# Kernel tuning notes

Measured on AMD Instinct MI355X. Metric: run time of the kernel, lower is better.

Reference implementation:

```python
import jax, jax.numpy as jnp
import numpy as np
from jax import lax

DN = ('NHWC', 'HWIO', 'NHWC')
N_MEM = 2000  # memory slots
BN_EPS = 1e-3


def _conv(x, w, b):
    # tf.nn.conv2d stride 2, SAME, NHWC / HWIO
    return lax.conv_general_dilated(x, w, (2, 2), 'SAME', dimension_numbers=DN) + b


def _convt(x, w, b):
    # tf.nn.conv2d_transpose; w is TF layout [kh, kw, out_ch, in_ch]
    return lax.conv_transpose(x, w, (2, 2), 'SAME', dimension_numbers=DN,
                              transpose_kernel=True) + b


def _bn(x, g, b):
    # BatchNormalization(training=True): batch statistics over N,H,W
    m = jnp.mean(x, axis=(0, 1, 2))
    v = jnp.var(x, axis=(0, 1, 2))
    return g * (x - m) * lax.rsqrt(v + BN_EPS) + b


def setup_inputs() -> dict:
    key = jax.random.key(0)
    ks = iter(jax.random.split(key, 40))
    def gn(shape, s=0.05):
        return jax.random.normal(next(ks), shape, jnp.float32) * s
    inp = {'x': jax.random.uniform(next(ks), (16, 256, 256, 3), jnp.float32)}
    inp.update(
        w_e1=gn((1, 1, 3, 16)), b_e1=gn((16,)),
        g_bn1=jnp.ones(16, jnp.float32), be_bn1=jnp.zeros(16, jnp.float32),
        w_e2=gn((3, 3, 16, 32)), b_e2=gn((32,)),
        g_bn2=jnp.ones(32, jnp.float32), be_bn2=jnp.zeros(32, jnp.float32),
        w_e3=gn((3, 3, 32, 64)), b_e3=gn((64,)),
        g_bn3=jnp.ones(64, jnp.float32), be_bn3=jnp.zeros(64, jnp.float32),
        w_mem=gn((1, 1, N_MEM, 64)),
        w_d1=gn((3, 3, 32, 64)), b_d1=gn((32,)),
        g_bnt1=jnp.ones(32, jnp.float32), be_bnt1=jnp.zeros(32, jnp.float32),
        w_d2=gn((3, 3, 16, 32)), b_d2=gn((16,)),
        g_bnt2=jnp.ones(16, jnp.float32), be_bnt2=jnp.zeros(16, jnp.float32),
        w_d3=gn((3, 3, 3, 16)), b_d3=gn((3,)),
    )
    return inp


def reference(x, w_e1, b_e1, g_bn1, be_bn1, w_e2, b_e2, g_bn2, be_bn2,
              w_e3, b_e3, g_bn3, be_bn3, w_mem,
              w_d1, b_d1, g_bnt1, be_bnt1, w_d2, b_d2, g_bnt2, be_bnt2,
              w_d3, b_d3):
    # ---- encode ----
    h = jax.nn.relu(_bn(_conv(x, w_e1, b_e1), g_bn1, be_bn1))   # [B,128,128,16]
    h = jax.nn.relu(_bn(_conv(h, w_e2, b_e2), g_bn2, be_bn2))   # [B,64,64,32]
    z = jax.nn.relu(_bn(_conv(h, w_e3, b_e3), g_bn3, be_bn3))   # [B,32,32,64]
    # ---- memory addressing ----
    mem = w_mem[0, 0]                                            # [N, 64]
    num = jnp.einsum('bhwc,nc->bhwn', z, mem)
    den = jnp.einsum('bhwc,nc->bhwn', z * z, mem * mem)
    att = jax.nn.softmax((num + 1e-12) / (den + 1e-12), axis=-1)  # [B,32,32,N]
    d = att - 1.0 / N_MEM                                        # hard shrinkage
    renorm = jnp.clip(jax.nn.relu(d) * att / (jnp.abs(d) + 1e-12),
                      1e-12, 1.0 - 1e-12)
    z_hat = jnp.einsum('bhwn,nc->bhwc', renorm, mem)             # [B,32,32,64]
    # ---- decode ----
    t = jax.nn.relu(_bn(_convt(z_hat, w_d1, b_d1), g_bnt1, be_bnt1))  # [B,64,64,32]
    t = jax.nn.relu(_bn(_convt(t, w_d2, b_d2), g_bnt2, be_bnt2))      # [B,128,128,16]
    x_hat = jnp.clip(_convt(t, w_d3, b_d3), 1e-12, 1.0 - 1e-12)       # [B,256,256,3]
    return x_hat
```

## Files before the change

### kernel.cpp

```cpp
#include <hip/hip_runtime.h>
#include <math.h>

typedef __bf16 bf16x8 __attribute__((ext_vector_type(8)));
typedef __bf16 bf16x4 __attribute__((ext_vector_type(4)));
typedef float  f32x16 __attribute__((ext_vector_type(16)));

static __device__ __forceinline__ f32x16 zero16() {
  f32x16 v;
  #pragma unroll
  for (int i = 0; i < 16; ++i) v[i] = 0.f;
  return v;
}
static __device__ __forceinline__ unsigned int bfbits(__bf16 b) {
  return (unsigned int)__builtin_bit_cast(unsigned short, b);
}
static __device__ __forceinline__ bf16x8 mk8(unsigned int a, unsigned int b,
                                             unsigned int c, unsigned int d) {
  uint4 t; t.x = a; t.y = b; t.z = c; t.w = d;
  return __builtin_bit_cast(bf16x8, t);
}

__global__ __launch_bounds__(256) void k_conv1(const float* __restrict__ x,
    const float* __restrict__ w, const float* __restrict__ b, float* __restrict__ y,
    float* __restrict__ partials) {
  int t = blockIdx.x*256 + threadIdx.x;
  int ox = t & 127, oy = (t >> 7) & 127, bb = t >> 14;
  const float* xp = x + ((size_t)((bb*256 + 2*oy)*256 + 2*ox))*3;
  float x0 = xp[0], x1 = xp[1], x2 = xp[2];
  float4 rg[4];
  float4* yp = (float4*)(y + (size_t)t*16);
  #pragma unroll
  for (int g = 0; g < 4; ++g) {
    float4 r;
    r.x = b[g*4+0] + x0*w[g*4+0] + x1*w[16+g*4+0] + x2*w[32+g*4+0];
    r.y = b[g*4+1] + x0*w[g*4+1] + x1*w[16+g*4+1] + x2*w[32+g*4+1];
    r.z = b[g*4+2] + x0*w[g*4+2] + x1*w[16+g*4+2] + x2*w[32+g*4+2];
    r.w = b[g*4+3] + x0*w[g*4+3] + x1*w[16+g*4+3] + x2*w[32+g*4+3];
    rg[g] = r;
    yp[g] = r;
  }
  float4 s4[4], q4[4];
  #pragma unroll
  for (int g=0; g<4; ++g) {
    s4[g] = rg[g];
    q4[g] = make_float4(rg[g].x*rg[g].x, rg[g].y*rg[g].y, rg[g].z*rg[g].z, rg[g].w*rg[g].w);
  }
  #pragma unroll
  for (int off=1; off<64; off<<=1) {
    #pragma unroll
    for (int g=0; g<4; ++g) {
      s4[g].x += __shfl_xor(s4[g].x, off); s4[g].y += __shfl_xor(s4[g].y, off);
      s4[g].z += __shfl_xor(s4[g].z, off); s4[g].w += __shfl_xor(s4[g].w, off);
      q4[g].x += __shfl_xor(q4[g].x, off); q4[g].y += __shfl_xor(q4[g].y, off);
      q4[g].z += __shfl_xor(q4[g].z, off); q4[g].w += __shfl_xor(q4[g].w, off);
    }
  }
  __shared__ float red[4][32];
  int wv = threadIdx.x >> 6, lane = threadIdx.x & 63;
  if (lane == 0) {
    #pragma unroll
    for (int g=0; g<4; ++g) {
      *(float4*)&red[wv][g*4]      = s4[g];
      *(float4*)&red[wv][16 + g*4] = q4[g];
    }
  }
  __syncthreads();
  if (threadIdx.x < 32)
    partials[(size_t)blockIdx.x*32 + threadIdx.x] =
      red[0][threadIdx.x]+red[1][threadIdx.x]+red[2][threadIdx.x]+red[3][threadIdx.x];
}

template<int C,int CSPLIT>
__global__ __launch_bounds__(256) void k_finalize2(const float* __restrict__ partials, int nblk,
    double inv_n, const float* __restrict__ g, const float* __restrict__ be, float* __restrict__ ss) {
  const int COUTT = C/CSPLIT;
  const int NSTAT = 2*C;
  const int PER = 256/NSTAT;
  __shared__ double red[256];
  int tid = threadIdx.x;
  int st = tid % NSTAT, sub = tid / NSTAT;
  int c = st % C, kind = st / C;
  int cq = c / COUTT, j = c % COUTT;
  int nb = nblk / CSPLIT;
  double acc = 0.0;
  #pragma unroll 4
  for (int i = sub; i < nb; i += PER) {
    int bq = cq + i*CSPLIT;
    acc += (double)partials[(size_t)bq*2*COUTT + kind*COUTT + j];
  }
  red[tid] = acc;
  __syncthreads();
  for (int off = PER>>1; off > 0; off >>= 1) {
    if (sub < off) red[tid] += red[tid + off*NSTAT];
    __syncthreads();
  }
  if (tid < C) {
    double mean = red[tid]*inv_n;
    double var  = red[C+tid]*inv_n - mean*mean;
    float scale = g[tid] * rsqrtf((float)var + 1e-3f);
    float shift = be[tid] - (float)mean*scale;
    ss[tid] = scale; ss[C+tid] = shift;
  }
}

template<int CIN,int COUT,int CSPLIT,int HIN,int HOUT,bool BN>
__global__ __launch_bounds__(256) void k_conv_bn(const float* __restrict__ in,
    const float* __restrict__ w, const float* __restrict__ bias,
    const float* __restrict__ ss, float* __restrict__ y, float* __restrict__ partials) {
  const int COUTT = COUT/CSPLIT;
  const int NW4 = COUTT/4;
  __shared__ float4 wlds[9*CIN*NW4];
  int bid = blockIdx.x;
  int cq  = bid % CSPLIT;
  int pxb = bid / CSPLIT;
  int c0  = cq*COUTT;
  for (int e = threadIdx.x; e < 9*CIN*NW4; e += 256) {
    int r = e / NW4, cg = e % NW4;
    wlds[e] = *(const float4*)(w + (size_t)r*COUT + c0 + cg*4);
  }
  __syncthreads();
  int t0 = pxb*256 + threadIdx.x;
  float4 acc[NW4];
  #pragma unroll
  for (int g=0; g<NW4; ++g) acc[g] = *(const float4*)(bias + c0 + g*4);
  int ox = t0 % HOUT, oy = (t0/HOUT) % HOUT, bb = t0/(HOUT*HOUT);
  #pragma unroll 1
  for (int dy=0; dy<3; ++dy) {
    #pragma unroll 1
    for (int dx=0; dx<3; ++dx) {
      int tap = dy*3+dx;
      int iy = 2*oy + dy, ix = 2*ox + dx;
      if (iy < HIN && ix < HIN) {
        const float* bp = in + ((size_t)(bb*HIN + iy)*HIN + ix)*CIN;
        #pragma unroll
        for (int ci4=0; ci4<CIN/4; ++ci4) {
          float4 v = *(const float4*)(bp + ci4*4);
          if (BN) {
            float4 sc = *(const float4*)(ss + ci4*4);
            float4 sh = *(const float4*)(ss + CIN + ci4*4);
            v.x = fmaxf(0.f, fmaf(v.x, sc.x, sh.x));
            v.y = fmaxf(0.f, fmaf(v.y, sc.y, sh.y));
            v.z = fmaxf(0.f, fmaf(v.z, sc.z, sh.z));
            v.w = fmaxf(0.f, fmaf(v.w, sc.w, sh.w));
          }
          float va[4] = {v.x, v.y, v.z, v.w};
          #pragma unroll
          for (int k=0;k<4;++k) {
            float vk = va[k];
            #pragma unroll
            for (int g=0; g<NW4; ++g) {
              float4 w4 = wlds[(tap*CIN + ci4*4 + k)*NW4 + g];
              acc[g].x = fmaf(vk, w4.x, acc[g].x);
              acc[g].y = fmaf(vk, w4.y, acc[g].y);
              acc[g].z = fmaf(vk, w4.z, acc[g].z);
              acc[g].w = fmaf(vk, w4.w, acc[g].w);
            }
          }
        }
      }
    }
  }
  float4* yp = (float4*)(y + (size_t)t0*COUT + c0);
  #pragma unroll
  for (int g=0;g<NW4;++g) yp[g] = acc[g];
  float4 s4[NW4], q4[NW4];
  #pragma unroll
  for (int g=0; g<NW4; ++g) {
    s4[g] = acc[g];
    q4[g] = make_float4(acc[g].x*acc[g].x, acc[g].y*acc[g].y,
                        acc[g].z*acc[g].z, acc[g].w*acc[g].w);
  }
  #pragma unroll
  for (int off=1; off<64; off<<=1) {
    #pragma unroll
    for (int g=0; g<NW4; ++g) {
      s4[g].x += __shfl_xor(s4[g].x, off); s4[g].y += __shfl_xor(s4[g].y, off);
      s4[g].z += __shfl_xor(s4[g].z, off); s4[g].w += __shfl_xor(s4[g].w, off);
      q4[g].x += __shfl_xor(q4[g].x, off); q4[g].y += __shfl_xor(q4[g].y, off);
      q4[g].z += __shfl_xor(q4[g].z, off); q4[g].w += __shfl_xor(q4[g].w, off);
    }
  }
  __shared__ float red[4][2*COUTT];
  int wv = threadIdx.x >> 6, lane = threadIdx.x & 63;
  if (lane == 0) {
    #pragma unroll
    for (int g=0; g<NW4; ++g) {
      *(float4*)&red[wv][g*4]         = s4[g];
      *(float4*)&red[wv][COUTT + g*4] = q4[g];
    }
  }
  __syncthreads();
  if (threadIdx.x < 2*COUTT)
    partials[(size_t)bid*2*COUTT + threadIdx.x] =
      red[0][threadIdx.x]+red[1][threadIdx.x]+red[2][threadIdx.x]+red[3][threadIdx.x];
}


__global__ __launch_bounds__(256) void k_prep_z(const float* __restrict__ y3,
    const float* __restrict__ ss,
    __bf16* __restrict__ ZH, __bf16* __restrict__ ZL,
    __bf16* __restrict__ Z2H, __bf16* __restrict__ Z2L) {
  int t = blockIdx.x*256 + threadIdx.x;
  float4 v = ((const float4*)y3)[t];
  int c0 = (t*4) & 63;
  float4 sc = *(const float4*)(ss + c0);
  float4 sh = *(const float4*)(ss + 64 + c0);
  float vv[4];
  vv[0] = fmaxf(0.f, fmaf(v.x, sc.x, sh.x));
  vv[1] = fmaxf(0.f, fmaf(v.y, sc.y, sh.y));
  vv[2] = fmaxf(0.f, fmaf(v.z, sc.z, sh.z));
  vv[3] = fmaxf(0.f, fmaf(v.w, sc.w, sh.w));
  bf16x4 h, l, h2, l2;
  #pragma unroll
  for (int i=0;i<4;++i) {
    float f = vv[i];
    __bf16 hb = (__bf16)f;
    h[i] = hb; l[i] = (__bf16)(f - (float)hb);
    float q = f*f;
    __bf16 qb = (__bf16)q;
    h2[i] = qb; l2[i] = (__bf16)(q - (float)qb);
  }
  ((bf16x4*)ZH)[t] = h;  ((bf16x4*)ZL)[t] = l;
  ((bf16x4*)Z2H)[t] = h2; ((bf16x4*)Z2L)[t] = l2;
}

__global__ __launch_bounds__(256) void k_prep_m(const float* __restrict__ mem,
    __bf16* __restrict__ MH, __bf16* __restrict__ ML,
    __bf16* __restrict__ M2H, __bf16* __restrict__ M2L,
    __bf16* __restrict__ MHT, __bf16* __restrict__ MLT) {
  int t = blockIdx.x*256 + threadIdx.x;
  int n = t >> 4, c0 = (t & 15)*4;
  float4 v = make_float4(0.f,0.f,0.f,0.f);
  if (n < 2000) v = *(const float4*)(mem + (size_t)n*64 + c0);
  float vv[4] = {v.x, v.y, v.z, v.w};
  bf16x4 h, l, h2, l2;
  #pragma unroll
  for (int i=0;i<4;++i) {
    float f = vv[i];
    __bf16 hb = (__bf16)f;
    h[i] = hb; l[i] = (__bf16)(f - (float)hb);
    float q = f*f;
    __bf16 qb = (__bf16)q;
    h2[i] = qb; l2[i] = (__bf16)(q - (float)qb);
  }
  *(bf16x4*)(MH  + (size_t)n*64 + c0) = h;
  *(bf16x4*)(ML  + (size_t)n*64 + c0) = l;
  *(bf16x4*)(M2H + (size_t)n*64 + c0) = h2;
  *(bf16x4*)(M2L + (size_t)n*64 + c0) = l2;
  #pragma unroll
  for (int i=0;i<4;++i) {
    MHT[(size_t)(c0+i)*2048 + n] = h[i];
    MLT[(size_t)(c0+i)*2048 + n] = l[i];
  }
}

__global__ __launch_bounds__(256) void k_pass1(
    const __bf16* __restrict__ ZH, const __bf16* __restrict__ ZL,
    const __bf16* __restrict__ Z2H, const __bf16* __restrict__ Z2L,
    const __bf16* __restrict__ MH, const __bf16* __restrict__ ML,
    const __bf16* __restrict__ M2H, const __bf16* __restrict__ M2L,
    float* __restrict__ S32, float* __restrict__ partM, float* __restrict__ partS) {
  int pb = blockIdx.x & 127, chunk = blockIdx.x >> 7;
  int wave = threadIdx.x >> 6, lane = threadIdx.x & 63;
  int p0 = pb*128 + wave*32;
  int col = lane & 31, hi = lane >> 5;
  bf16x8 bzh[4], bzl[4], b2h[4], b2l[4];
  size_t zoff = (size_t)(p0 + col)*64 + hi*8;
  #pragma unroll
  for (int ks=0;ks<4;++ks) {
    bzh[ks] = *(const bf16x8*)(ZH  + zoff + ks*16);
    bzl[ks] = *(const bf16x8*)(ZL  + zoff + ks*16);
    b2h[ks] = *(const bf16x8*)(Z2H + zoff + ks*16);
    b2l[ks] = *(const bf16x8*)(Z2L + zoff + ks*16);
  }
  float m = -3.4e38f, S = 0.f;
  int nbase = chunk*256;
  #pragma unroll 2
  for (int t=0; t<8; ++t) {
    int n0 = nbase + t*32;
    size_t arow = (size_t)(n0 + col)*64 + hi*8;
    f32x16 num = zero16(), den = zero16();
    #pragma unroll
    for (int ks=0;ks<4;++ks) {
      bf16x8 amh = *(const bf16x8*)(MH + arow + ks*16);
      bf16x8 aml = *(const bf16x8*)(ML + arow + ks*16);
      num = __builtin_amdgcn_mfma_f32_32x32x16_bf16(amh, bzh[ks], num, 0,0,0);
      num = __builtin_amdgcn_mfma_f32_32x32x16_bf16(amh, bzl[ks], num, 0,0,0);
      num = __builtin_amdgcn_mfma_f32_32x32x16_bf16(aml, bzh[ks], num, 0,0,0);
      bf16x8 a2h = *(const bf16x8*)(M2H + arow + ks*16);
      bf16x8 a2l = *(const bf16x8*)(M2L + arow + ks*16);
      den = __builtin_amdgcn_mfma_f32_32x32x16_bf16(a2h, b2h[ks], den, 0,0,0);
      den = __builtin_amdgcn_mfma_f32_32x32x16_bf16(a2h, b2l[ks], den, 0,0,0);
      den = __builtin_amdgcn_mfma_f32_32x32x16_bf16(a2l, b2h[ks], den, 0,0,0);
    }
    bool maskt = (n0 + 32 > 2000);
    float sv[16];
    float tmax = -3.4e38f;
    #pragma unroll
    for (int r=0;r<16;++r) {
      float s = (num[r] + 1e-12f) * __builtin_amdgcn_rcpf(den[r] + 1e-12f);
      if (maskt) {
        int nn = n0 + (r&3) + 8*(r>>2) + 4*hi;
        if (nn >= 2000) s = -3.4e38f;
      }
      sv[r] = s;
      tmax = fmaxf(tmax, s);
    }
    {
      size_t sbase = ((size_t)((chunk*8 + t)*16384 + p0 + col)*2 + hi)*16;
      *(float4*)(S32 + sbase)      = make_float4(sv[0], sv[1], sv[2], sv[3]);
      *(float4*)(S32 + sbase + 4)  = make_float4(sv[4], sv[5], sv[6], sv[7]);
      *(float4*)(S32 + sbase + 8)  = make_float4(sv[8], sv[9], sv[10], sv[11]);
      *(float4*)(S32 + sbase + 12) = make_float4(sv[12], sv[13], sv[14], sv[15]);
    }
    float mn = fmaxf(m, tmax);
    float ssum = 0.f;
    #pragma unroll
    for (int r=0;r<16;++r) ssum += __expf(sv[r] - mn);
    S = S*__expf(m - mn) + ssum;
    m = mn;
  }
  float mo = __shfl_xor(m, 32);
  float So = __shfl_xor(S, 32);
  float mf = fmaxf(m, mo);
  float Sf = S*__expf(m - mf) + So*__expf(mo - mf);
  if (lane < 32) {
    int p = p0 + col;
    partM[chunk*16384 + p] = mf;
    partS[chunk*16384 + p] = Sf;
  }
}

__global__ __launch_bounds__(256) void k_pass2(
    const float* __restrict__ S32,
    const __bf16* __restrict__ MHT, const __bf16* __restrict__ MLT,
    const float* __restrict__ partM, const float* __restrict__ partS,
    float* __restrict__ ZP) {
  int pb = blockIdx.x & 127, chunk = blockIdx.x >> 7;
  int wave = threadIdx.x >> 6, lane = threadIdx.x & 63;
  int p0 = pb*128 + wave*32;
  int col = lane & 31, hi = lane >> 5;
  int p = p0 + col;
  float pmv[8];
  float Mp = -3.4e38f;
  #pragma unroll
  for (int c=0;c<8;++c) { pmv[c] = partM[c*16384 + p]; Mp = fmaxf(Mp, pmv[c]); }
  float Ssum = 0.f;
  #pragma unroll
  for (int c=0;c<8;++c) Ssum += partS[c*16384 + p] * __expf(pmv[c] - Mp);
  float CM  = Mp + __logf(Ssum);
  float thr = CM - 7.6009025f;
  f32x16 za0 = zero16(), za1 = zero16();
  int nbase = chunk*256;
  #pragma unroll 2
  for (int t=0; t<8; ++t) {
    int n0 = nbase + t*32;
    size_t sbase = ((size_t)((chunk*8 + t)*16384 + p)*2 + hi)*16;
    float4 sq0 = *(const float4*)(S32 + sbase);
    float4 sq1 = *(const float4*)(S32 + sbase + 4);
    float4 sq2 = *(const float4*)(S32 + sbase + 8);
    float4 sq3 = *(const float4*)(S32 + sbase + 12);
    float sv[16] = {sq0.x,sq0.y,sq0.z,sq0.w, sq1.x,sq1.y,sq1.z,sq1.w,
                    sq2.x,sq2.y,sq2.z,sq2.w, sq3.x,sq3.y,sq3.z,sq3.w};
    float rv[16];
    #pragma unroll
    for (int r=0;r<16;++r) {
      float s = sv[r];
      float att = __expf(s - CM);
      rv[r] = (s > thr) ? att : 0.f;
    }
    unsigned int qh[8];
    #pragma unroll
    for (int qd=0; qd<4; ++qd) {
      #pragma unroll
      for (int pr=0; pr<2; ++pr) {
        float r0 = rv[qd*4 + pr*2], r1 = rv[qd*4 + pr*2 + 1];
        qh[qd*2+pr] = bfbits((__bf16)r0) | (bfbits((__bf16)r1) << 16);
      }
    }
    unsigned int qhp[8];
    #pragma unroll
    for (int i=0;i<8;++i) qhp[i] = (unsigned int)__shfl_xor((int)qh[i], 32);
    bf16x8 f1h = hi ? mk8(qhp[2],qhp[3],qh[2],qh[3]) : mk8(qh[0],qh[1],qhp[0],qhp[1]);
    bf16x8 f2h = hi ? mk8(qhp[6],qhp[7],qh[6],qh[7]) : mk8(qh[4],qh[5],qhp[4],qhp[5]);
    #pragma unroll
    for (int kh=0; kh<2; ++kh) {
      bf16x8 fh = kh ? f2h : f1h;
      size_t bofs = (size_t)col*2048 + n0 + kh*16 + hi*8;
      bf16x8 bmh0 = *(const bf16x8*)(MHT + bofs);
      bf16x8 bml0 = *(const bf16x8*)(MLT + bofs);
      bf16x8 bmh1 = *(const bf16x8*)(MHT + bofs + (size_t)32*2048);
      bf16x8 bml1 = *(const bf16x8*)(MLT + bofs + (size_t)32*2048);
      za0 = __builtin_amdgcn_mfma_f32_32x32x16_bf16(fh, bmh0, za0, 0,0,0);
      za0 = __builtin_amdgcn_mfma_f32_32x32x16_bf16(fh, bml0, za0, 0,0,0);
      za1 = __builtin_amdgcn_mfma_f32_32x32x16_bf16(fh, bmh1, za1, 0,0,0);
      za1 = __builtin_amdgcn_mfma_f32_32x32x16_bf16(fh, bml1, za1, 0,0,0);
    }
  }
  size_t base = (size_t)chunk << 20;
  #pragma unroll
  for (int r=0;r<16;++r) {
    int prow = (r&3) + 8*(r>>2) + 4*hi;
    size_t o = base + (size_t)(p0 + prow)*64 + col;
    ZP[o]      = za0[r];
    ZP[o + 32] = za1[r];
  }
}

__global__ __launch_bounds__(256) void k_zcomb(const float* __restrict__ ZP,
                                               float* __restrict__ Gz) {
  int t = blockIdx.x*256 + threadIdx.x;
  float a = 0.f;
  #pragma unroll
  for (int c=0;c<8;++c) a += ZP[(size_t)c*1048576 + t];
  Gz[t] = a;
}

template<int CIN,int COUT,int CSPLIT,int HIN,bool BN>
__global__ __launch_bounds__(256) void k_convt_bn(const float* __restrict__ in,
    const float* __restrict__ w, const float* __restrict__ bias,
    const float* __restrict__ ss, float* __restrict__ y, float* __restrict__ partials) {
  const int COUTT = COUT/CSPLIT;
  const int HOUT = 2*HIN;
  __shared__ float4 wlds[4*COUTT*(CIN/4)];
  int bid = blockIdx.x;
  int cq = bid % CSPLIT; int rest = bid / CSPLIT;
  int cls = rest % 4;    int pxb = rest / 4;
  int pm = cls >> 1, pn = cls & 1;
  int c0 = cq*COUTT;
  int NTI = (pm == 0) ? 2 : 1;
  int NTJ = (pn == 0) ? 2 : 1;
  int NT = NTI*NTJ;
  for (int e = threadIdx.x; e < NT*COUTT*(CIN/4); e += 256) {
    int tl = e / (COUTT*(CIN/4));
    int rem = e % (COUTT*(CIN/4));
    int cc = rem / (CIN/4), ci4 = rem % (CIN/4);
    int ki = pm + 2*(tl / NTJ), kj = pn + 2*(tl % NTJ);
    wlds[e] = *(const float4*)(w + ((size_t)(ki*3+kj)*COUT + c0 + cc)*CIN + ci4*4);
  }
  __syncthreads();
  int t0 = pxb*256 + threadIdx.x;
  float acc[COUTT];
  #pragma unroll
  for (int cc=0;cc<COUTT;++cc) acc[cc] = bias[c0+cc];
  int nx = t0 % HIN, my = (t0/HIN) % HIN, bb = t0/(HIN*HIN);
  #pragma unroll 1
  for (int ti=0; ti<NTI; ++ti) {
    #pragma unroll 1
    for (int tj=0; tj<NTJ; ++tj) {
      int tl = ti*NTJ + tj;
      int i = my - ti, j = nx - tj;
      if (i >= 0 && j >= 0) {
        const float* bp = in + ((size_t)(bb*HIN + i)*HIN + j)*CIN;
        #pragma unroll
        for (int ci4=0; ci4<CIN/4; ++ci4) {
          float4 v = *(const float4*)(bp + ci4*4);
          if (BN) {
            float4 sc = *(const float4*)(ss + ci4*4);
            float4 sh = *(const float4*)(ss + CIN + ci4*4);
            v.x = fmaxf(0.f, fmaf(v.x, sc.x, sh.x));
            v.y = fmaxf(0.f, fmaf(v.y, sc.y, sh.y));
            v.z = fmaxf(0.f, fmaf(v.z, sc.z, sh.z));
            v.w = fmaxf(0.f, fmaf(v.w, sc.w, sh.w));
          }
          #pragma unroll
          for (int cc=0;cc<COUTT;++cc) {
            float4 w4 = wlds[(tl*COUTT + cc)*(CIN/4) + ci4];
            float a = acc[cc];
            a = fmaf(v.x, w4.x, a);
            a = fmaf(v.y, w4.y, a);
            a = fmaf(v.z, w4.z, a);
            a = fmaf(v.w, w4.w, a);
            acc[cc] = a;
          }
        }
      }
    }
  }
  int m = 2*my + pm, n = 2*nx + pn;
  float* yp = y + ((size_t)(bb*HOUT + m)*HOUT + n)*COUT + c0;
  #pragma unroll
  for (int g=0;g<COUTT/4;++g)
    ((float4*)yp)[g] = make_float4(acc[g*4], acc[g*4+1], acc[g*4+2], acc[g*4+3]);
  float s[COUTT], q[COUTT];
  #pragma unroll
  for (int cc=0;cc<COUTT;++cc) { s[cc] = acc[cc]; q[cc] = acc[cc]*acc[cc]; }
  #pragma unroll
  for (int off=1; off<64; off<<=1) {
    #pragma unroll
    for (int cc=0;cc<COUTT;++cc) {
      s[cc] += __shfl_xor(s[cc], off);
      q[cc] += __shfl_xor(q[cc], off);
    }
  }
  __shared__ float red[4][2*COUTT];
  int wv = threadIdx.x >> 6, lane = threadIdx.x & 63;
  if (lane == 0) {
    #pragma unroll
    for (int cc=0;cc<COUTT;++cc) { red[wv][cc] = s[cc]; red[wv][COUTT+cc] = q[cc]; }
  }
  __syncthreads();
  if (threadIdx.x < 2*COUTT)
    partials[(size_t)bid*2*COUTT + threadIdx.x] =
      red[0][threadIdx.x]+red[1][threadIdx.x]+red[2][threadIdx.x]+red[3][threadIdx.x];
}

__global__ __launch_bounds__(256) void k_convt_final(const float* __restrict__ in,
    const float* __restrict__ w, const float* __restrict__ bias,
    const float* __restrict__ ss, float* __restrict__ out) {
  const int CIN=16, HIN=128, HOUT=256;
  __shared__ float4 wlds[4*3*4];
  int cls = blockIdx.x & 3;
  int pxb = blockIdx.x >> 2;
  int pm = cls >> 1, pn = cls & 1;
  int NTI = (pm == 0) ? 2 : 1;
  int NTJ = (pn == 0) ? 2 : 1;
  int NT = NTI*NTJ;
  if (threadIdx.x < NT*3*4) {
    int e = threadIdx.x;
    int tl = e / 12, rem = e % 12;
    int c = rem / 4, ci4 = rem % 4;
    int ki = pm + 2*(tl / NTJ), kj = pn + 2*(tl % NTJ);
    wlds[e] = *(const float4*)(w + ((size_t)(ki*3+kj)*3 + c)*CIN + ci4*4);
  }
  __syncthreads();
  int t = pxb*256 + threadIdx.x;
  int nx = t % HIN, my = (t/HIN) % HIN, bb = t/(HIN*HIN);
  float a0 = bias[0], a1 = bias[1], a2 = bias[2];
  #pragma unroll 1
  for (int ti=0; ti<NTI; ++ti) {
    #pragma unroll 1
    for (int tj=0; tj<NTJ; ++tj) {
      int tl = ti*NTJ + tj;
      int i = my - ti, j = nx - tj;
      if (i >= 0 && j >= 0) {
        const float* bp = in + ((size_t)(bb*HIN + i)*HIN + j)*CIN;
        #pragma unroll
        for (int ci4=0; ci4<4; ++ci4) {
          float4 v = *(const float4*)(bp + ci4*4);
          float4 sc = *(const float4*)(ss + ci4*4);
          float4 sh = *(const float4*)(ss + CIN + ci4*4);
          v.x = fmaxf(0.f, fmaf(v.x, sc.x, sh.x));
          v.y = fmaxf(0.f, fmaf(v.y, sc.y, sh.y));
          v.z = fmaxf(0.f, fmaf(v.z, sc.z, sh.z));
          v.w = fmaxf(0.f, fmaf(v.w, sc.w, sh.w));
          float4 w0 = wlds[(tl*3 + 0)*4 + ci4];
          float4 w1 = wlds[(tl*3 + 1)*4 + ci4];
          float4 w2 = wlds[(tl*3 + 2)*4 + ci4];
          a0 = fmaf(v.x, w0.x, a0); a0 = fmaf(v.y, w0.y, a0);
          a0 = fmaf(v.z, w0.z, a0); a0 = fmaf(v.w, w0.w, a0);
          a1 = fmaf(v.x, w1.x, a1); a1 = fmaf(v.y, w1.y, a1);
          a1 = fmaf(v.z, w1.z, a1); a1 = fmaf(v.w, w1.w, a1);
          a2 = fmaf(v.x, w2.x, a2); a2 = fmaf(v.y, w2.y, a2);
          a2 = fmaf(v.z, w2.z, a2); a2 = fmaf(v.w, w2.w, a2);
        }
      }
    }
  }
  int m = 2*my + pm, n = 2*nx + pn;
  float* op = out + ((size_t)(bb*HOUT + m)*HOUT + n)*3;
  op[0] = fminf(fmaxf(a0, 1e-12f), 1.0f);
  op[1] = fminf(fmaxf(a1, 1e-12f), 1.0f);
  op[2] = fminf(fmaxf(a2, 1e-12f), 1.0f);
}

extern "C" void kernel_launch(void* const* d_in, const int* in_sizes, int n_in,
                              void* d_out, int out_size, void* d_ws, size_t ws_size,
                              hipStream_t stream) {
  const float* x    = (const float*)d_in[0];
  const float* w_e1 = (const float*)d_in[1];
  const float* b_e1 = (const float*)d_in[2];
  const float* g1   = (const float*)d_in[3];
  const float* be1  = (const float*)d_in[4];
  const float* w_e2 = (const float*)d_in[5];
  const float* b_e2 = (const float*)d_in[6];
  const float* g2   = (const float*)d_in[7];
  const float* be2  = (const float*)d_in[8];
  const float* w_e3 = (const float*)d_in[9];
  const float* b_e3 = (const float*)d_in[10];
  const float* g3   = (const float*)d_in[11];
  const float* be3  = (const float*)d_in[12];
  const float* wmem = (const float*)d_in[13];
  const float* w_d1 = (const float*)d_in[14];
  const float* b_d1 = (const float*)d_in[15];
  const float* gt1  = (const float*)d_in[16];
  const float* bet1 = (const float*)d_in[17];
  const float* w_d2 = (const float*)d_in[18];
  const float* b_d2 = (const float*)d_in[19];
  const float* gt2  = (const float*)d_in[20];
  const float* bet2 = (const float*)d_in[21];
  const float* w_d3 = (const float*)d_in[22];
  const float* b_d3 = (const float*)d_in[23];
  float* out = (float*)d_out;

  float* ws = (float*)d_ws;
  float* S32 = ws;
  float* A   = ws;
  float* Cc  = ws + 4194304;
  float* Gz  = ws + 33554432;
  float* ZP  = Gz + 1048576;
  float* E   = ZP + 8388608;
  float* bfbase = E + 1048576;
  __bf16* ZH  = (__bf16*)bfbase;
  __bf16* ZL  = ZH  + 16384*64;
  __bf16* Z2H = ZL  + 16384*64;
  __bf16* Z2L = Z2H + 16384*64;
  __bf16* MH  = Z2L + 16384*64;
  __bf16* ML  = MH  + 2048*64;
  __bf16* M2H = ML  + 2048*64;
  __bf16* M2L = M2H + 2048*64;
  __bf16* MHT = M2L + 2048*64;
  __bf16* MLT = MHT + 64*2048;
  float* PT   = (float*)(MLT + 64*2048);
  float* SS   = PT + 131072;
  float* PM   = SS + 256;
  float* PS   = PM + 131072;
  (void)ws_size; (void)in_sizes; (void)n_in; (void)out_size;

  k_conv1<<<1024,256,0,stream>>>(x, w_e1, b_e1, A, PT);
  k_finalize2<16,1><<<1,256,0,stream>>>(PT, 1024, 1.0/262144.0, g1, be1, SS);
  k_conv_bn<16,32,2,128,64,true><<<512,256,0,stream>>>(A, w_e2, b_e2, SS, Cc, PT);
  k_finalize2<32,2><<<1,256,0,stream>>>(PT, 512, 1.0/65536.0, g2, be2, SS);
  k_conv_bn<32,64,8,64,32,true><<<512,256,0,stream>>>(Cc, w_e3, b_e3, SS, E, PT);
  k_finalize2<64,8><<<1,256,0,stream>>>(PT, 512, 1.0/16384.0, g3, be3, SS);
  k_prep_m<<<128,256,0,stream>>>(wmem, MH, ML, M2H, M2L, MHT, MLT);
  k_prep_z<<<1024,256,0,stream>>>(E, SS, ZH, ZL, Z2H, Z2L);
  k_pass1<<<1024,256,0,stream>>>(ZH, ZL, Z2H, Z2L, MH, ML, M2H, M2L, S32, PM, PS);
  k_pass2<<<1024,256,0,stream>>>(S32, MHT, MLT, PM, PS, ZP);
  k_zcomb<<<4096,256,0,stream>>>(ZP, Gz);
  k_convt_bn<64,32,2,32,false><<<512,256,0,stream>>>(Gz, w_d1, b_d1, nullptr, Cc, PT);
  k_finalize2<32,2><<<1,256,0,stream>>>(PT, 512, 1.0/65536.0, gt1, bet1, SS);
  k_convt_bn<32,16,1,64,true><<<1024,256,0,stream>>>(Cc, w_d2, b_d2, SS, A, PT);
  k_finalize2<16,1><<<1,256,0,stream>>>(PT, 1024, 1.0/262144.0, gt2, bet2, SS);
  k_convt_final<<<4096,256,0,stream>>>(A, w_d3, b_d3, SS, out);
}
```

Measured before the change: 385.9 us.

## Store bf16 exponentials plus per-tile max instead of fp32 scores between softmax passes

Pass1 now writes exp(s - running max) as bf16 together with a per-tile max, instead of writing the raw fp32 scores. Pass2 rescales these by exp(mt - CM) and applies the shrinkage threshold in the scaled domain. This halves the large intermediate buffer traffic and removes an exp per element in pass2. Both kernels also move to one 64-thread wave per block with 4x more blocks. The intermediate values lose precision because they are rounded to bf16 before rescaling, though they were already rounded to bf16 before the MFMA.

```diff
diff --git a/kernel.cpp b/kernel.cpp
--- a/kernel.cpp
+++ b/kernel.cpp
@@ -254,15 +254,16 @@
   }
 }
 
-__global__ __launch_bounds__(256) void k_pass1(
+__global__ __launch_bounds__(64) void k_pass1(
     const __bf16* __restrict__ ZH, const __bf16* __restrict__ ZL,
     const __bf16* __restrict__ Z2H, const __bf16* __restrict__ Z2L,
     const __bf16* __restrict__ MH, const __bf16* __restrict__ ML,
     const __bf16* __restrict__ M2H, const __bf16* __restrict__ M2L,
-    float* __restrict__ S32, float* __restrict__ partM, float* __restrict__ partS) {
-  int pb = blockIdx.x & 127, chunk = blockIdx.x >> 7;
-  int wave = threadIdx.x >> 6, lane = threadIdx.x & 63;
-  int p0 = pb*128 + wave*32;
+    __bf16* __restrict__ U, float* __restrict__ MT,
+    float* __restrict__ partM, float* __restrict__ partS) {
+  int pb = blockIdx.x & 511, chunk = blockIdx.x >> 9;
+  int lane = threadIdx.x;
+  int p0 = pb*32;
   int col = lane & 31, hi = lane >> 5;
   bf16x8 bzh[4], bzl[4], b2h[4], b2l[4];
   size_t zoff = (size_t)(p0 + col)*64 + hi*8;
@@ -306,19 +307,24 @@
       sv[r] = s;
       tmax = fmaxf(tmax, s);
     }
-    {
-      size_t sbase = ((size_t)((chunk*8 + t)*16384 + p0 + col)*2 + hi)*16;
-      *(float4*)(S32 + sbase)      = make_float4(sv[0], sv[1], sv[2], sv[3]);
-      *(float4*)(S32 + sbase + 4)  = make_float4(sv[4], sv[5], sv[6], sv[7]);
-      *(float4*)(S32 + sbase + 8)  = make_float4(sv[8], sv[9], sv[10], sv[11]);
-      *(float4*)(S32 + sbase + 12) = make_float4(sv[12], sv[13], sv[14], sv[15]);
-    }
     float mn = fmaxf(m, tmax);
     float ssum = 0.f;
-    #pragma unroll
-    for (int r=0;r<16;++r) ssum += __expf(sv[r] - mn);
+    unsigned int up[8];
+    #pragma unroll
+    for (int j=0;j<8;++j) {
+      float u0 = __expf(sv[2*j]   - mn);
+      float u1 = __expf(sv[2*j+1] - mn);
+      ssum += u0; ssum += u1;
+      up[j] = bfbits((__bf16)u0) | (bfbits((__bf16)u1) << 16);
+    }
     S = S*__expf(m - mn) + ssum;
     m = mn;
+    size_t idx = (size_t)((chunk*8 + t)*16384 + p0 + col)*2 + hi;
+    uint4 st0; st0.x = up[0]; st0.y = up[1]; st0.z = up[2]; st0.w = up[3];
+    uint4 st1; st1.x = up[4]; st1.y = up[5]; st1.z = up[6]; st1.w = up[7];
+    *(uint4*)(U + idx*16)     = st0;
+    *(uint4*)(U + idx*16 + 8) = st1;
+    MT[idx] = mn;
   }
   float mo = __shfl_xor(m, 32);
   float So = __shfl_xor(S, 32);
@@ -331,14 +337,14 @@
   }
 }
 
-__global__ __launch_bounds__(256) void k_pass2(
-    const float* __restrict__ S32,
+__global__ __launch_bounds__(64) void k_pass2(
+    const __bf16* __restrict__ U, const float* __restrict__ MT,
     const __bf16* __restrict__ MHT, const __bf16* __restrict__ MLT,
     const float* __restrict__ partM, const float* __restrict__ partS,
     float* __restrict__ ZP) {
-  int pb = blockIdx.x & 127, chunk = blockIdx.x >> 7;
-  int wave = threadIdx.x >> 6, lane = threadIdx.x & 63;
-  int p0 = pb*128 + wave*32;
+  int pb = blockIdx.x & 511, chunk = blockIdx.x >> 9;
+  int lane = threadIdx.x;
+  int p0 = pb*32;
   int col = lane & 31, hi = lane >> 5;
   int p = p0 + col;
   float pmv[8];
@@ -355,28 +361,21 @@
   #pragma unroll 2
   for (int t=0; t<8; ++t) {
     int n0 = nbase + t*32;
-    size_t sbase = ((size_t)((chunk*8 + t)*16384 + p)*2 + hi)*16;
-    float4 sq0 = *(const float4*)(S32 + sbase);
-    float4 sq1 = *(const float4*)(S32 + sbase + 4);
-    float4 sq2 = *(const float4*)(S32 + sbase + 8);
-    float4 sq3 = *(const float4*)(S32 + sbase + 12);
-    float sv[16] = {sq0.x,sq0.y,sq0.z,sq0.w, sq1.x,sq1.y,sq1.z,sq1.w,
-                    sq2.x,sq2.y,sq2.z,sq2.w, sq3.x,sq3.y,sq3.z,sq3.w};
-    float rv[16];
-    #pragma unroll
-    for (int r=0;r<16;++r) {
-      float s = sv[r];
-      float att = __expf(s - CM);
-      rv[r] = (s > thr) ? att : 0.f;
-    }
+    size_t idx = (size_t)((chunk*8 + t)*16384 + p)*2 + hi;
+    uint4 a = *(const uint4*)(U + idx*16);
+    uint4 b = *(const uint4*)(U + idx*16 + 8);
+    float mt = MT[idx];
+    float scale = __expf(mt - CM);
+    float thru  = __expf(thr - mt);
+    unsigned int ua[8] = {a.x,a.y,a.z,a.w,b.x,b.y,b.z,b.w};
     unsigned int qh[8];
     #pragma unroll
-    for (int qd=0; qd<4; ++qd) {
-      #pragma unroll
-      for (int pr=0; pr<2; ++pr) {
-        float r0 = rv[qd*4 + pr*2], r1 = rv[qd*4 + pr*2 + 1];
-        qh[qd*2+pr] = bfbits((__bf16)r0) | (bfbits((__bf16)r1) << 16);
-      }
+    for (int j=0;j<8;++j) {
+      float u0 = __builtin_bit_cast(float, ua[j] << 16);
+      float u1 = __builtin_bit_cast(float, ua[j] & 0xffff0000u);
+      float r0 = (u0 > thru) ? u0*scale : 0.f;
+      float r1 = (u1 > thru) ? u1*scale : 0.f;
+      qh[j] = bfbits((__bf16)r0) | (bfbits((__bf16)r1) << 16);
     }
     unsigned int qhp[8];
     #pragma unroll
@@ -594,10 +593,10 @@
   float* out = (float*)d_out;
 
   float* ws = (float*)d_ws;
-  float* S32 = ws;
+  __bf16* U  = (__bf16*)ws;
   float* A   = ws;
   float* Cc  = ws + 4194304;
-  float* Gz  = ws + 33554432;
+  float* Gz  = ws + 16777216;
   float* ZP  = Gz + 1048576;
   float* E   = ZP + 8388608;
   float* bfbase = E + 1048576;
@@ -615,6 +614,7 @@
   float* SS   = PT + 131072;
   float* PM   = SS + 256;
   float* PS   = PM + 131072;
+  float* MT   = PS + 131072;
   (void)ws_size; (void)in_sizes; (void)n_in; (void)out_size;
 
   k_conv1<<<1024,256,0,stream>>>(x, w_e1, b_e1, A, PT);
@@ -625,8 +625,8 @@
   k_finalize2<64,8><<<1,256,0,stream>>>(PT, 512, 1.0/16384.0, g3, be3, SS);
   k_prep_m<<<128,256,0,stream>>>(wmem, MH, ML, M2H, M2L, MHT, MLT);
   k_prep_z<<<1024,256,0,stream>>>(E, SS, ZH, ZL, Z2H, Z2L);
-  k_pass1<<<1024,256,0,stream>>>(ZH, ZL, Z2H, Z2L, MH, ML, M2H, M2L, S32, PM, PS);
-  k_pass2<<<1024,256,0,stream>>>(S32, MHT, MLT, PM, PS, ZP);
+  k_pass1<<<4096,64,0,stream>>>(ZH, ZL, Z2H, Z2L, MH, ML, M2H, M2L, U, MT, PM, PS);
+  k_pass2<<<4096,64,0,stream>>>(U, MT, MHT, MLT, PM, PS, ZP);
   k_zcomb<<<4096,256,0,stream>>>(ZP, Gz);
   k_convt_bn<64,32,2,32,false><<<512,256,0,stream>>>(Gz, w_d1, b_d1, nullptr, Cc, PT);
   k_finalize2<32,2><<<1,256,0,stream>>>(PT, 512, 1.0/65536.0, gt1, bet1, SS);
```

New measurement: 362.8 us. -6.0%, faster.
